# Performance work log

Hardware: AMD Instinct MI355X
Metric: run time of the kernel (lower is better)

Reference implementation:

```python
import jax, jax.numpy as jnp
import numpy as np
from jax import lax

DN = ('NCHW', 'OIHW', 'NCHW')

def _conv(x, w, b, stride, pad):
    o = lax.conv_general_dilated(x, w, (stride, stride), [(pad, pad), (pad, pad)], dimension_numbers=DN)
    return o + b[None, :, None, None]

def _conv_transpose(x, w, b, stride, pad):
    # w in torch ConvTranspose2d layout [Cin, Cout, kh, kw]
    k = w.shape[2]
    wf = jnp.flip(w, (2, 3)).transpose(1, 0, 2, 3)  # -> [Cout, Cin, kh, kw]
    p = k - 1 - pad
    o = lax.conv_general_dilated(x, wf, (1, 1), [(p, p), (p, p)], lhs_dilation=(stride, stride), dimension_numbers=DN)
    return o + b[None, :, None, None]

def setup_inputs() -> dict:
    key = jax.random.key(0)
    ks = jax.random.split(key, 16)
    s = 0.05
    NUM_EMB, EMB_DIM = 512, 128
    inp = {
        'x': jax.random.normal(ks[0], (32, 1, 224, 224), jnp.float32),
        # encoder
        'w_e1': jax.random.normal(ks[1], (64, 1, 4, 4), jnp.float32) * s,
        'b_e1': jnp.zeros((64,), jnp.float32),
        'w_e2': jax.random.normal(ks[2], (128, 64, 4, 4), jnp.float32) * s,
        'b_e2': jnp.zeros((128,), jnp.float32),
        'w_e3': jax.random.normal(ks[3], (128, 128, 3, 3), jnp.float32) * s,
        'b_e3': jnp.zeros((128,), jnp.float32),
        # codebook (torch init: uniform(-1/K, 1/K))
        'emb': jax.random.uniform(ks[4], (NUM_EMB, EMB_DIM), jnp.float32, -1.0 / NUM_EMB, 1.0 / NUM_EMB),
        # decoder
        'w_d1': jax.random.normal(ks[5], (128, 128, 3, 3), jnp.float32) * s,
        'b_d1': jnp.zeros((128,), jnp.float32),
        'w_dt1': jax.random.normal(ks[6], (128, 64, 4, 4), jnp.float32) * s,  # ConvTranspose [Cin,Cout,k,k]
        'b_dt1': jnp.zeros((64,), jnp.float32),
        'w_dt2': jax.random.normal(ks[7], (64, 1, 4, 4), jnp.float32) * s,
        'b_dt2': jnp.zeros((1,), jnp.float32),
    }
    return inp

def reference(x, w_e1, b_e1, w_e2, b_e2, w_e3, b_e3, emb, w_d1, b_d1, w_dt1, b_dt1, w_dt2, b_dt2):
    sg = lax.stop_gradient
    # --- encoder ---
    h = jax.nn.relu(_conv(x, w_e1, b_e1, 2, 1))
    h = jax.nn.relu(_conv(h, w_e2, b_e2, 2, 1))
    z_e = _conv(h, w_e3, b_e3, 1, 1)  # [B,128,H/4,W/4]
    B, C, H, W = z_e.shape
    # --- vector quantizer (faithful to source, incl. missing -2*z@e.T cross term) ---
    z_flat = z_e.transpose(0, 2, 3, 1).reshape(-1, C)  # [BHW, C]
    distances = (z_flat ** 2).sum(1, keepdims=True) + (emb ** 2).sum(1)  # [BHW, K]
    indices = jnp.argmin(distances, axis=1)
    z_q = emb[indices].reshape(B, H, W, C).transpose(0, 3, 1, 2)
    codebook_loss = jnp.mean((z_q - sg(z_e)) ** 2)
    commitment_loss = jnp.mean((sg(z_q) - z_e) ** 2)
    vq_loss = codebook_loss + commitment_loss
    # --- decoder ---
    d = _conv(z_q, w_d1, b_d1, 1, 1)
    d = jax.nn.relu(_conv_transpose(d, w_dt1, b_dt1, 2, 1))
    reconstructed_x = _conv_transpose(d, w_dt2, b_dt2, 2, 1)
    reconstruction_loss = jnp.mean((reconstructed_x - x) ** 2)
    total_loss = reconstruction_loss + vq_loss
    return (reconstructed_x, total_loss, reconstruction_loss, vq_loss)
```

## Files before the change

kernel.cpp:

```cpp
#include <hip/hip_runtime.h>
#include <hip/hip_bf16.h>

using bf16 = __hip_bfloat16;
using short8 = __attribute__((ext_vector_type(8))) short;
using f32x16 = __attribute__((ext_vector_type(16))) float;

__device__ __forceinline__ ushort f2us(float v) {
    bf16 h = __float2bfloat16(v);
    return *reinterpret_cast<ushort*>(&h);
}

#define MFMA32(a, b, c) __builtin_amdgcn_mfma_f32_32x32x16_bf16((a), (b), (c), 0, 0, 0)

__device__ __forceinline__ void gload16(const void* g, void* l) {
    __builtin_amdgcn_global_load_lds(
        (const __attribute__((address_space(1))) unsigned int*)g,
        (__attribute__((address_space(3))) unsigned int*)l, 16, 0, 0);
}

__device__ __forceinline__ int cls8(int i) {
    if (i == 0) return 0;
    if (i == 1) return 1;
    if (i == 2) return 2;
    if (i == 109) return 5;
    if (i == 110) return 6;
    if (i == 111) return 7;
    return (i & 1) ? 4 : 3;
}

__global__ void k_codebook(const float* __restrict__ emb, float* __restrict__ c) {
    __shared__ float sval[512];
    __shared__ int   sidx[512];
    int k = threadIdx.x;
    float s = 0.f;
    const float4* e4 = (const float4*)(emb + k * 128);
    #pragma unroll
    for (int d = 0; d < 32; ++d) {
        float4 v = e4[d];
        s += v.x * v.x + v.y * v.y + v.z * v.z + v.w * v.w;
    }
    sval[k] = s; sidx[k] = k;
    __syncthreads();
    for (int off = 256; off > 0; off >>= 1) {
        if (k < off) {
            float v2 = sval[k + off]; int i2 = sidx[k + off];
            if (v2 < sval[k] || (v2 == sval[k] && i2 < sidx[k])) { sval[k] = v2; sidx[k] = i2; }
        }
        __syncthreads();
    }
    int kmin = sidx[0];
    if (k < 128) c[k] = emb[kmin * 128 + k];
}

__global__ __launch_bounds__(256) void k_prepack(const float* __restrict__ w_e2,
                                                 const float* __restrict__ w_e3,
                                                 ushort* __restrict__ Wb2f,
                                                 ushort* __restrict__ Wb3f) {
    int i = blockIdx.x * 256 + threadIdx.x;
    const int n2 = 131072;
    const int n3 = 147456;
    if (i < n2) {
        int j = i & 7, l = (i >> 3) & 63, ks = (i >> 9) & 3, mf = (i >> 11) & 1,
            mh = (i >> 12) & 1, tap = i >> 13;
        int co = mh * 64 + mf * 32 + (l & 31);
        int ci = ks * 16 + (l >> 5) * 8 + j;
        int kh = tap >> 2, kw = tap & 3;
        Wb2f[i] = f2us(w_e2[((co * 64 + ci) * 4 + kh) * 4 + kw]);
    } else if (i < n2 + n3) {
        int t = i - n2;
        int j = t & 7, l = (t >> 3) & 63, ks = (t >> 9) & 7, mf = (t >> 12) & 1,
            mh = (t >> 13) & 1, tap = t >> 14;
        int co = mh * 64 + mf * 32 + (l & 31);
        int ci = ks * 16 + (l >> 5) * 8 + j;
        int kh = tap / 3, kw = tap % 3;
        Wb3f[t] = f2us(w_e3[((co * 128 + ci) * 3 + kh) * 3 + kw]);
    }
}

__global__ __launch_bounds__(256) void k_conv1(const float* __restrict__ x,
                                               const float* __restrict__ w,
                                               const float* __restrict__ bias,
                                               ushort* __restrict__ h1s) {
    __shared__ float wl[1024];
    __shared__ float bl[64];
    __shared__ __align__(16) char obuf[28672];
    int tid = threadIdx.x;
    for (int i = tid; i < 1024; i += 256) wl[i] = w[i];
    if (tid < 64) bl[tid] = bias[tid];
    __syncthreads();
    int r = blockIdx.x, b = blockIdx.y;
    int g = tid >> 6;
    int q = tid & 63;
    bool act = q < 56;
    int oh = 2 * r + (q >= 28);
    int ow0 = (q % 28) * 4;

    float xv[4][10];
    const float* xb = x + (size_t)b * 50176;
    #pragma unroll
    for (int kh = 0; kh < 4; ++kh) {
        int ih = 2 * oh - 1 + kh;
        bool rok = act && (unsigned)ih < 224u;
        #pragma unroll
        for (int j = 0; j < 10; ++j) {
            int iw = 2 * ow0 - 1 + j;
            xv[kh][j] = (rok && (unsigned)iw < 224u) ? xb[ih * 224 + iw] : 0.f;
        }
    }
    float a[4][16];
    #pragma unroll
    for (int i = 0; i < 4; ++i)
        #pragma unroll
        for (int j = 0; j < 16; ++j) a[i][j] = 0.f;

    const float4* wl4 = (const float4*)wl;
    #pragma unroll
    for (int j = 0; j < 16; ++j) {
        int co = g * 16 + j;
        #pragma unroll
        for (int kh = 0; kh < 4; ++kh) {
            float4 wr = wl4[co * 4 + kh];
            #pragma unroll
            for (int i = 0; i < 4; ++i) {
                a[i][j] += xv[kh][2*i+0]*wr.x + xv[kh][2*i+1]*wr.y
                         + xv[kh][2*i+2]*wr.z + xv[kh][2*i+3]*wr.w;
            }
        }
    }
    if (act) {
        #pragma unroll
        for (int i = 0; i < 4; ++i) {
            int ow = ow0 + i, wq = ow >> 1, pw = ow & 1;
            char* rowb = obuf + (oh & 1) * 14336 + wq * 256;
            int key = (wq & 15) << 4;
            #pragma unroll
            for (int j = 0; j < 16; ++j) {
                int co = g * 16 + j;
                *(ushort*)(rowb + ((pw * 128 + co * 2) ^ key)) =
                    f2us(fmaxf(a[i][j] + bl[co], 0.f));
            }
        }
    }
    __syncthreads();
    const float4* sb = (const float4*)obuf;
    for (int i = tid; i < 1792; i += 256) {
        int ph = (i >= 896) ? 1 : 0;
        float4* dst = (float4*)((char*)h1s + (((size_t)(b * 2 + ph)) * 56 + r) * 14336);
        dst[i - ph * 896] = sb[i];
    }
}

__global__ __launch_bounds__(256) void k_conv2_mfma(const ushort* __restrict__ h1s,
                                                    const ushort* __restrict__ Wb2f,
                                                    const float* __restrict__ bias,
                                                    ushort* __restrict__ h2s) {
    __shared__ __align__(16) char ldsc[6 * 14848 + 2 * 16384];
    int lin = blockIdx.x;
    int v = (lin & 7) * 112 + (lin >> 3);
    int b = v / 28, oh0 = (v % 28) * 2;
    int tid = threadIdx.x, lane = tid & 63, wv = tid >> 6;
    int mh = wv & 1, r = wv >> 1;
    int lrow = lane & 31, khalf = lane >> 5;
    const float4 z4 = {0.f, 0.f, 0.f, 0.f};

    if (tid < 192) {
        int s = tid >> 5, rr = (tid >> 4) & 1, col = tid & 15;
        ((float4*)(ldsc + s * 14848 + rr * 57 * 256))[col] = z4;
    }
    #pragma unroll
    for (int s = 0; s < 6; ++s) {
        int ph = (s < 3) ? 0 : 1;
        int rr = (s < 3) ? (oh0 + s) : (oh0 - 4 + s);
        char* ldst = ldsc + s * 14848 + 256;
        if ((unsigned)rr < 56u) {
            const char* src = (const char*)h1s + (((size_t)(b * 2 + ph)) * 56 + rr) * 14336;
            for (int c2 = wv; c2 < 14; c2 += 4)
                gload16(src + c2 * 1024 + lane * 16, ldst + c2 * 1024);
        } else {
            for (int i = tid; i < 896; i += 256) ((float4*)ldst)[i] = z4;
        }
    }
    {
        const char* asrc = (const char*)Wb2f;
        #pragma unroll
        for (int t = 0; t < 4; ++t)
            gload16(asrc + (wv * 4 + t) * 1024 + lane * 16,
                    ldsc + 89088 + (wv * 4 + t) * 1024);
    }
    __syncthreads();

    const f32x16 vz = {0,0,0,0,0,0,0,0,0,0,0,0,0,0,0,0};
    f32x16 acc[2][2];
    #pragma unroll
    for (int cf = 0; cf < 2; ++cf)
        #pragma unroll
        for (int mf = 0; mf < 2; ++mf) acc[cf][mf] = vz;

    #pragma unroll
    for (int tap = 0; tap < 16; ++tap) {
        const char* Acur = ldsc + 89088 + (tap & 1) * 16384;
        if (tap < 15) {
            char* Anxt = ldsc + 89088 + ((tap + 1) & 1) * 16384;
            const char* asrc = (const char*)Wb2f + (size_t)(tap + 1) * 16384;
            #pragma unroll
            for (int t = 0; t < 4; ++t)
                gload16(asrc + (wv * 4 + t) * 1024 + lane * 16,
                        Anxt + (wv * 4 + t) * 1024);
        }
        short8 af[2][4];
        #pragma unroll
        for (int mf = 0; mf < 2; ++mf)
            #pragma unroll
            for (int ks = 0; ks < 4; ++ks)
                af[mf][ks] = *(const short8*)(Acur + ((mh * 2 + mf) * 4 + ks) * 1024 + lane * 16);
        const int kh = tap >> 2, kw = tap & 3;
        const int pw = (kw & 1) ? 0 : 1;
        const int wofs = (kw == 0) ? 0 : (kw == 3) ? 2 : 1;
        const int sbase = (kh == 0) ? 3 : (kh == 1) ? 0 : (kh == 2) ? 4 : 1;
        const char* slab = ldsc + (sbase + r) * 14848;
        const int colb = pw * 128 + khalf * 16;
        #pragma unroll
        for (int cf = 0; cf < 2; ++cf) {
            int wp = cf * 24 + lrow + wofs;
            int key = ((wp - 1) & 15) << 4;
            const char* rowb = slab + wp * 256;
            #pragma unroll
            for (int ks = 0; ks < 4; ++ks) {
                short8 bv = *(const short8*)(rowb + ((colb + ks * 32) ^ key));
                acc[cf][0] = MFMA32(af[0][ks], bv, acc[cf][0]);
                acc[cf][1] = MFMA32(af[1][ks], bv, acc[cf][1]);
            }
        }
        __syncthreads();
    }
    {
        char* obuf = ldsc + r * 14336;
        #pragma unroll
        for (int cf = 0; cf < 2; ++cf) {
            int ow = cf * 24 + lrow;
            if (cf == 0 || lrow >= 8) {
                char* rowb = obuf + ow * 256;
                int key = (ow & 15) << 4;
                #pragma unroll
                for (int mf = 0; mf < 2; ++mf)
                    #pragma unroll
                    for (int reg = 0; reg < 16; ++reg) {
                        int co = mh * 64 + mf * 32 + (reg & 3) + 8 * (reg >> 2) + 4 * khalf;
                        float vv = fmaxf(acc[cf][mf][reg] + bias[co], 0.f);
                        *(ushort*)(rowb + ((co * 2) ^ key)) = f2us(vv);
                    }
            }
        }
    }
    __syncthreads();
    const float4* sb = (const float4*)ldsc;
    for (int i = tid; i < 1792; i += 256) {
        int rr = (i >= 896) ? 1 : 0;
        float4* dst = (float4*)((char*)h2s + ((size_t)(b * 56) + oh0 + rr) * 14336);
        dst[i - rr * 896] = sb[i];
    }
}

__global__ __launch_bounds__(512, 2) void k_conv3_mfma(const ushort* __restrict__ h2s,
                                                       const ushort* __restrict__ Wb3f,
                                                       const float* __restrict__ bias,
                                                       const float* __restrict__ c,
                                                       float* __restrict__ vq_part) {
    __shared__ __align__(16) char ldsc[6 * 14848 + 2 * 32768];
    __shared__ float red[8];
    int lin = blockIdx.x;
    int v = (lin & 7) * 56 + (lin >> 3);
    int b = v / 14, oh0 = (v % 14) * 4;
    int tid = threadIdx.x, lane = tid & 63, wv = tid >> 6;
    int mh = wv & 1, r = wv >> 1;
    int lrow = lane & 31, khalf = lane >> 5;
    const float4 z4 = {0.f, 0.f, 0.f, 0.f};

    if (tid < 192) {
        int s = tid >> 5, rr = (tid >> 4) & 1, col = tid & 15;
        ((float4*)(ldsc + s * 14848 + rr * 57 * 256))[col] = z4;
    }
    #pragma unroll
    for (int s = 0; s < 6; ++s) {
        int rr = oh0 - 1 + s;
        char* ldst = ldsc + s * 14848 + 256;
        if ((unsigned)rr < 56u) {
            const char* src = (const char*)h2s + ((size_t)b * 56 + rr) * 14336;
            for (int c2 = wv; c2 < 14; c2 += 8)
                gload16(src + c2 * 1024 + lane * 16, ldst + c2 * 1024);
        } else {
            for (int i = tid; i < 896; i += 512) ((float4*)ldst)[i] = z4;
        }
    }
    {
        const char* asrc = (const char*)Wb3f;
        #pragma unroll
        for (int t = 0; t < 4; ++t)
            gload16(asrc + (wv * 4 + t) * 1024 + lane * 16,
                    ldsc + 89088 + (wv * 4 + t) * 1024);
    }
    __syncthreads();

    const f32x16 vz = {0,0,0,0,0,0,0,0,0,0,0,0,0,0,0,0};
    f32x16 acc[2][2];
    #pragma unroll
    for (int cf = 0; cf < 2; ++cf)
        #pragma unroll
        for (int mf = 0; mf < 2; ++mf) acc[cf][mf] = vz;

    #pragma unroll
    for (int tap = 0; tap < 9; ++tap) {
        const char* Acur = ldsc + 89088 + (tap & 1) * 32768;
        if (tap < 8) {
            char* Anxt = ldsc + 89088 + ((tap + 1) & 1) * 32768;
            const char* asrc = (const char*)Wb3f + (size_t)(tap + 1) * 32768;
            #pragma unroll
            for (int t = 0; t < 4; ++t)
                gload16(asrc + (wv * 4 + t) * 1024 + lane * 16,
                        Anxt + (wv * 4 + t) * 1024);
        }
        short8 af[2][8];
        #pragma unroll
        for (int mf = 0; mf < 2; ++mf)
            #pragma unroll
            for (int ks = 0; ks < 8; ++ks)
                af[mf][ks] = *(const short8*)(Acur + ((mh * 2 + mf) * 8 + ks) * 1024 + lane * 16);
        const int kh = tap / 3, kw = tap % 3;
        const char* slab = ldsc + (r + kh) * 14848;
        #pragma unroll
        for (int cf = 0; cf < 2; ++cf) {
            int wp = cf * 24 + lrow + kw;
            int key = ((wp - 1) & 15) << 4;
            const char* rowb = slab + wp * 256;
            #pragma unroll
            for (int ks = 0; ks < 8; ++ks) {
                short8 bv = *(const short8*)(rowb + ((khalf * 16 + ks * 32) ^ key));
                acc[cf][0] = MFMA32(af[0][ks], bv, acc[cf][0]);
                acc[cf][1] = MFMA32(af[1][ks], bv, acc[cf][1]);
            }
        }
        __syncthreads();
    }
    float ls = 0.f;
    #pragma unroll
    for (int cf = 0; cf < 2; ++cf) {
        if (cf == 0 || lrow >= 8) {
            #pragma unroll
            for (int mf = 0; mf < 2; ++mf)
                #pragma unroll
                for (int reg = 0; reg < 16; ++reg) {
                    int co = mh * 64 + mf * 32 + (reg & 3) + 8 * (reg >> 2) + 4 * khalf;
                    float z = acc[cf][mf][reg] + bias[co];
                    float d = c[co] - z;
                    ls += d * d;
                }
        }
    }
    #pragma unroll
    for (int off = 32; off > 0; off >>= 1) ls += __shfl_down(ls, off);
    if (lane == 0) red[wv] = ls;
    __syncthreads();
    if (tid == 0) {
        float t = 0.f;
        #pragma unroll
        for (int i = 0; i < 8; ++i) t += red[i];
        vq_part[v] = t;
    }
}

__global__ __launch_bounds__(128) void k_SD3(const float* __restrict__ w_d1,
                                             const float* __restrict__ c,
                                             const float* __restrict__ b_d1,
                                             float* __restrict__ D3) {
    int co = blockIdx.x, ci = threadIdx.x;
    __shared__ float cl[128];
    __shared__ float part[9][128];
    cl[ci] = c[ci];
    __syncthreads();
    const float* wp = w_d1 + (co * 128 + ci) * 9;
    float cv = cl[ci];
    #pragma unroll
    for (int t = 0; t < 9; ++t) part[t][ci] = wp[t] * cv;
    __syncthreads();
    for (int off = 64; off > 0; off >>= 1) {
        if (ci < off) {
            #pragma unroll
            for (int t = 0; t < 9; ++t) part[t][ci] += part[t][ci + off];
        }
        __syncthreads();
    }
    if (ci < 9) {
        int rh = ci / 3, rw = ci % 3;
        int kh0 = (rh == 0) ? 1 : 0, kh1 = (rh == 2) ? 1 : 2;
        int kw0 = (rw == 0) ? 1 : 0, kw1 = (rw == 2) ? 1 : 2;
        float a = b_d1[co];
        for (int kh = kh0; kh <= kh1; ++kh)
            for (int kw = kw0; kw <= kw1; ++kw)
                a += part[kh * 3 + kw][0];
        D3[co * 9 + ci] = a;
    }
}

__global__ __launch_bounds__(64) void k_d2c(const float* __restrict__ D3,
                                            const float* __restrict__ w_dt1,
                                            const float* __restrict__ b_dt1,
                                            float* __restrict__ d2c) {
    __shared__ float dl[1152];
    int gh = blockIdx.x, gw = blockIdx.y, co2 = threadIdx.x;
    for (int i = co2; i < 1152; i += 64) dl[i] = D3[i];
    __syncthreads();
    const int rep[8] = {0, 1, 2, 4, 3, 109, 110, 111};
    int oh = rep[gh], ow = rep[gw];
    float a = b_dt1[co2];
    #pragma unroll
    for (int th = 0; th < 2; ++th) {
        int kh = ((oh + 1) & 1) + 2 * th;
        int ih = (oh + 1 - kh) >> 1;
        if ((unsigned)ih >= 56u) continue;
        int rh = (ih == 0) ? 0 : (ih == 55) ? 2 : 1;
        #pragma unroll
        for (int tw = 0; tw < 2; ++tw) {
            int kw = ((ow + 1) & 1) + 2 * tw;
            int iw = (ow + 1 - kw) >> 1;
            if ((unsigned)iw >= 56u) continue;
            int rw = (iw == 0) ? 0 : (iw == 55) ? 2 : 1;
            float t = 0.f;
            for (int ci = 0; ci < 128; ++ci)
                t += dl[ci * 9 + rh * 3 + rw] * w_dt1[(ci * 64 + co2) * 16 + kh * 4 + kw];
            a += t;
        }
    }
    d2c[(gh * 8 + gw) * 64 + co2] = fmaxf(a, 0.f);
}

__global__ __launch_bounds__(256) void k_Rbuild(const float* __restrict__ d2c,
                                                const float* __restrict__ w_dt2,
                                                const float* __restrict__ b_dt2,
                                                float* __restrict__ R) {
    __shared__ float el[1024];
    int tid = threadIdx.x;
    #pragma unroll
    for (int q = 0; q < 4; ++q) {
        int id = tid * 4 + q;
        int kh = id >> 8, kw = (id >> 6) & 3, gh = (id >> 3) & 7, gw = id & 7;
        float t = 0.f;
        const float* dp = d2c + (gh * 8 + gw) * 64;
        const float* wp = w_dt2 + kh * 4 + kw;
        for (int ci = 0; ci < 64; ++ci) t += dp[ci] * wp[ci * 16];
        el[((kh * 4 + kw) * 8 + gh) * 8 + gw] = t;
    }
    __syncthreads();
    int s = blockIdx.x * 256 + tid;
    int oh = s / 224, ow = s % 224;
    float a = b_dt2[0];
    #pragma unroll
    for (int th = 0; th < 2; ++th) {
        int kh = ((oh + 1) & 1) + 2 * th;
        int ih = (oh + 1 - kh) >> 1;
        if ((unsigned)ih >= 112u) continue;
        int ch = cls8(ih);
        #pragma unroll
        for (int tw = 0; tw < 2; ++tw) {
            int kw = ((ow + 1) & 1) + 2 * tw;
            int iw = (ow + 1 - kw) >> 1;
            if ((unsigned)iw >= 112u) continue;
            int cw = cls8(iw);
            a += el[((kh * 4 + kw) * 8 + ch) * 8 + cw];
        }
    }
    R[s] = a;
}

__global__ __launch_bounds__(256) void k_out(const float* __restrict__ R,
                                             const float* __restrict__ x,
                                             float* __restrict__ out,
                                             float* __restrict__ rec_part) {
    int base = blockIdx.x * 512 + threadIdx.x;
    float v = 0.f;
    #pragma unroll
    for (int t = 0; t < 2; ++t) {
        int i4 = base + t * 256;
        int s4 = i4 % 12544;
        float4 r = ((const float4*)R)[s4];
        float4 xv = ((const float4*)x)[i4];
        ((float4*)out)[i4] = r;
        float dx = r.x - xv.x, dy = r.y - xv.y, dz = r.z - xv.z, dw = r.w - xv.w;
        v += dx * dx + dy * dy + dz * dz + dw * dw;
    }
    __shared__ float red[4];
    #pragma unroll
    for (int off = 32; off > 0; off >>= 1) v += __shfl_down(v, off);
    int wid = threadIdx.x >> 6, lane = threadIdx.x & 63;
    if (lane == 0) red[wid] = v;
    __syncthreads();
    if (threadIdx.x == 0) rec_part[blockIdx.x] = red[0] + red[1] + red[2] + red[3];
}

__global__ __launch_bounds__(256) void k_fin(const float* __restrict__ vq_part,
                                             const float* __restrict__ rec_part,
                                             float* __restrict__ out, int loss_base) {
    __shared__ float sv[256], sr[256];
    float a = 0.f, b2 = 0.f;
    for (int i = threadIdx.x; i < 448; i += 256) a  += vq_part[i];
    for (int i = threadIdx.x; i < 784; i += 256) b2 += rec_part[i];
    sv[threadIdx.x] = a; sr[threadIdx.x] = b2;
    __syncthreads();
    for (int off = 128; off > 0; off >>= 1) {
        if (threadIdx.x < off) { sv[threadIdx.x] += sv[threadIdx.x + off]; sr[threadIdx.x] += sr[threadIdx.x + off]; }
        __syncthreads();
    }
    if (threadIdx.x == 0) {
        float vq  = 2.f * sv[0] / 12845056.f;
        float rec = sr[0] / 1605632.f;
        out[loss_base + 0] = rec + vq;
        out[loss_base + 1] = rec;
        out[loss_base + 2] = vq;
    }
}

extern "C" void kernel_launch(void* const* d_in, const int* in_sizes, int n_in,
                              void* d_out, int out_size, void* d_ws, size_t ws_size,
                              hipStream_t stream) {
    const float* x     = (const float*)d_in[0];
    const float* w_e1  = (const float*)d_in[1];
    const float* b_e1  = (const float*)d_in[2];
    const float* w_e2  = (const float*)d_in[3];
    const float* b_e2  = (const float*)d_in[4];
    const float* w_e3  = (const float*)d_in[5];
    const float* b_e3  = (const float*)d_in[6];
    const float* emb   = (const float*)d_in[7];
    const float* w_d1  = (const float*)d_in[8];
    const float* b_d1  = (const float*)d_in[9];
    const float* w_dt1 = (const float*)d_in[10];
    const float* b_dt1 = (const float*)d_in[11];
    const float* w_dt2 = (const float*)d_in[12];
    const float* b_dt2 = (const float*)d_in[13];
    float* out = (float*)d_out;
    float* ws  = (float*)d_ws;

    float* c        = ws + 16;
    float* D3       = ws + 256;
    float* d2c      = ws + 2048;
    float* R        = ws + 8192;
    float* vq_part  = ws + 65536;
    float* rec_part = ws + 67584;
    ushort* Wb2f    = (ushort*)(ws + 131072);
    ushort* Wb3f    = (ushort*)(ws + 196608);
    ushort* h1s     = (ushort*)(ws + 1310720);
    ushort* h2s     = (ushort*)(ws + 14155776);

    k_codebook<<<1, 512, 0, stream>>>(emb, c);
    k_prepack<<<1088, 256, 0, stream>>>(w_e2, w_e3, Wb2f, Wb3f);
    k_conv1<<<dim3(56, 32), 256, 0, stream>>>(x, w_e1, b_e1, h1s);
    k_conv2_mfma<<<896, 256, 0, stream>>>(h1s, Wb2f, b_e2, h2s);
    k_conv3_mfma<<<448, 512, 0, stream>>>(h2s, Wb3f, b_e3, c, vq_part);
    k_SD3<<<128, 128, 0, stream>>>(w_d1, c, b_d1, D3);
    k_d2c<<<dim3(8, 8), 64, 0, stream>>>(D3, w_dt1, b_dt1, d2c);
    k_Rbuild<<<196, 256, 0, stream>>>(d2c, w_dt2, b_dt2, R);
    k_out<<<784, 256, 0, stream>>>(R, x, out, rec_part);
    k_fin<<<1, 256, 0, stream>>>(vq_part, rec_part, out, out_size - 3);
}
```

Measured before the change: 185.7 us.

## Shrink conv2/conv3 blocks to one output row and single-buffer weights

```diff
diff --git a/kernel.cpp b/kernel.cpp
--- a/kernel.cpp
+++ b/kernel.cpp
@@ -154,23 +154,24 @@
                                                     const ushort* __restrict__ Wb2f,
                                                     const float* __restrict__ bias,
                                                     ushort* __restrict__ h2s) {
-    __shared__ __align__(16) char ldsc[6 * 14848 + 2 * 16384];
+    __shared__ __align__(16) char ldsc[4 * 14848 + 16384];
+    char* Ab = ldsc + 4 * 14848;
     int lin = blockIdx.x;
-    int v = (lin & 7) * 112 + (lin >> 3);
-    int b = v / 28, oh0 = (v % 28) * 2;
+    int v = (lin & 7) * 224 + (lin >> 3);
+    int b = v / 56, oh = v % 56;
     int tid = threadIdx.x, lane = tid & 63, wv = tid >> 6;
-    int mh = wv & 1, r = wv >> 1;
+    int mh = wv & 1, cf = wv >> 1;
     int lrow = lane & 31, khalf = lane >> 5;
     const float4 z4 = {0.f, 0.f, 0.f, 0.f};
 
-    if (tid < 192) {
+    if (tid < 128) {
         int s = tid >> 5, rr = (tid >> 4) & 1, col = tid & 15;
         ((float4*)(ldsc + s * 14848 + rr * 57 * 256))[col] = z4;
     }
     #pragma unroll
-    for (int s = 0; s < 6; ++s) {
-        int ph = (s < 3) ? 0 : 1;
-        int rr = (s < 3) ? (oh0 + s) : (oh0 - 4 + s);
+    for (int s = 0; s < 4; ++s) {
+        int ph = s >> 1;
+        int rr = (s == 0) ? oh : (s == 1) ? oh + 1 : (s == 2) ? oh - 1 : oh;
         char* ldst = ldsc + s * 14848 + 256;
         if ((unsigned)rr < 56u) {
             const char* src = (const char*)h1s + (((size_t)(b * 2 + ph)) * 56 + rr) * 14336;
@@ -181,191 +182,159 @@
         }
     }
     {
-        const char* asrc = (const char*)Wb2f;
         #pragma unroll
         for (int t = 0; t < 4; ++t)
-            gload16(asrc + (wv * 4 + t) * 1024 + lane * 16,
-                    ldsc + 89088 + (wv * 4 + t) * 1024);
+            gload16((const char*)Wb2f + (wv * 4 + t) * 1024 + lane * 16,
+                    Ab + (wv * 4 + t) * 1024);
     }
     __syncthreads();
 
     const f32x16 vz = {0,0,0,0,0,0,0,0,0,0,0,0,0,0,0,0};
-    f32x16 acc[2][2];
-    #pragma unroll
-    for (int cf = 0; cf < 2; ++cf)
-        #pragma unroll
-        for (int mf = 0; mf < 2; ++mf) acc[cf][mf] = vz;
+    f32x16 acc0 = vz, acc1 = vz;
 
     #pragma unroll
     for (int tap = 0; tap < 16; ++tap) {
-        const char* Acur = ldsc + 89088 + (tap & 1) * 16384;
+        short8 af[2][4];
+        #pragma unroll
+        for (int mf = 0; mf < 2; ++mf)
+            #pragma unroll
+            for (int ks = 0; ks < 4; ++ks)
+                af[mf][ks] = *(const short8*)(Ab + ((mh * 2 + mf) * 4 + ks) * 1024 + lane * 16);
+        __syncthreads();
         if (tap < 15) {
-            char* Anxt = ldsc + 89088 + ((tap + 1) & 1) * 16384;
             const char* asrc = (const char*)Wb2f + (size_t)(tap + 1) * 16384;
             #pragma unroll
             for (int t = 0; t < 4; ++t)
                 gload16(asrc + (wv * 4 + t) * 1024 + lane * 16,
-                        Anxt + (wv * 4 + t) * 1024);
-        }
-        short8 af[2][4];
-        #pragma unroll
-        for (int mf = 0; mf < 2; ++mf)
-            #pragma unroll
-            for (int ks = 0; ks < 4; ++ks)
-                af[mf][ks] = *(const short8*)(Acur + ((mh * 2 + mf) * 4 + ks) * 1024 + lane * 16);
+                        Ab + (wv * 4 + t) * 1024);
+        }
         const int kh = tap >> 2, kw = tap & 3;
         const int pw = (kw & 1) ? 0 : 1;
         const int wofs = (kw == 0) ? 0 : (kw == 3) ? 2 : 1;
-        const int sbase = (kh == 0) ? 3 : (kh == 1) ? 0 : (kh == 2) ? 4 : 1;
-        const char* slab = ldsc + (sbase + r) * 14848;
+        const int sidx = (kh == 0) ? 2 : (kh == 1) ? 0 : (kh == 2) ? 3 : 1;
+        const char* slab = ldsc + sidx * 14848;
         const int colb = pw * 128 + khalf * 16;
-        #pragma unroll
-        for (int cf = 0; cf < 2; ++cf) {
-            int wp = cf * 24 + lrow + wofs;
-            int key = ((wp - 1) & 15) << 4;
-            const char* rowb = slab + wp * 256;
-            #pragma unroll
-            for (int ks = 0; ks < 4; ++ks) {
-                short8 bv = *(const short8*)(rowb + ((colb + ks * 32) ^ key));
-                acc[cf][0] = MFMA32(af[0][ks], bv, acc[cf][0]);
-                acc[cf][1] = MFMA32(af[1][ks], bv, acc[cf][1]);
-            }
+        int wp = cf * 24 + lrow + wofs;
+        int key = ((wp - 1) & 15) << 4;
+        const char* rowb = slab + wp * 256;
+        #pragma unroll
+        for (int ks = 0; ks < 4; ++ks) {
+            short8 bv = *(const short8*)(rowb + ((colb + ks * 32) ^ key));
+            acc0 = MFMA32(af[0][ks], bv, acc0);
+            acc1 = MFMA32(af[1][ks], bv, acc1);
         }
         __syncthreads();
     }
     {
-        char* obuf = ldsc + r * 14336;
-        #pragma unroll
-        for (int cf = 0; cf < 2; ++cf) {
-            int ow = cf * 24 + lrow;
-            if (cf == 0 || lrow >= 8) {
-                char* rowb = obuf + ow * 256;
-                int key = (ow & 15) << 4;
-                #pragma unroll
-                for (int mf = 0; mf < 2; ++mf)
-                    #pragma unroll
-                    for (int reg = 0; reg < 16; ++reg) {
-                        int co = mh * 64 + mf * 32 + (reg & 3) + 8 * (reg >> 2) + 4 * khalf;
-                        float vv = fmaxf(acc[cf][mf][reg] + bias[co], 0.f);
-                        *(ushort*)(rowb + ((co * 2) ^ key)) = f2us(vv);
-                    }
-            }
-        }
-    }
-    __syncthreads();
-    const float4* sb = (const float4*)ldsc;
-    for (int i = tid; i < 1792; i += 256) {
-        int rr = (i >= 896) ? 1 : 0;
-        float4* dst = (float4*)((char*)h2s + ((size_t)(b * 56) + oh0 + rr) * 14336);
-        dst[i - rr * 896] = sb[i];
-    }
-}
-
-__global__ __launch_bounds__(512, 2) void k_conv3_mfma(const ushort* __restrict__ h2s,
-                                                       const ushort* __restrict__ Wb3f,
-                                                       const float* __restrict__ bias,
-                                                       const float* __restrict__ c,
-                                                       float* __restrict__ vq_part) {
-    __shared__ __align__(16) char ldsc[6 * 14848 + 2 * 32768];
-    __shared__ float red[8];
-    int lin = blockIdx.x;
-    int v = (lin & 7) * 56 + (lin >> 3);
-    int b = v / 14, oh0 = (v % 14) * 4;
-    int tid = threadIdx.x, lane = tid & 63, wv = tid >> 6;
-    int mh = wv & 1, r = wv >> 1;
-    int lrow = lane & 31, khalf = lane >> 5;
-    const float4 z4 = {0.f, 0.f, 0.f, 0.f};
-
-    if (tid < 192) {
-        int s = tid >> 5, rr = (tid >> 4) & 1, col = tid & 15;
-        ((float4*)(ldsc + s * 14848 + rr * 57 * 256))[col] = z4;
-    }
-    #pragma unroll
-    for (int s = 0; s < 6; ++s) {
-        int rr = oh0 - 1 + s;
-        char* ldst = ldsc + s * 14848 + 256;
-        if ((unsigned)rr < 56u) {
-            const char* src = (const char*)h2s + ((size_t)b * 56 + rr) * 14336;
-            for (int c2 = wv; c2 < 14; c2 += 8)
-                gload16(src + c2 * 1024 + lane * 16, ldst + c2 * 1024);
-        } else {
-            for (int i = tid; i < 896; i += 512) ((float4*)ldst)[i] = z4;
-        }
-    }
-    {
-        const char* asrc = (const char*)Wb3f;
-        #pragma unroll
-        for (int t = 0; t < 4; ++t)
-            gload16(asrc + (wv * 4 + t) * 1024 + lane * 16,
-                    ldsc + 89088 + (wv * 4 + t) * 1024);
-    }
-    __syncthreads();
-
-    const f32x16 vz = {0,0,0,0,0,0,0,0,0,0,0,0,0,0,0,0};
-    f32x16 acc[2][2];
-    #pragma unroll
-    for (int cf = 0; cf < 2; ++cf)
-        #pragma unroll
-        for (int mf = 0; mf < 2; ++mf) acc[cf][mf] = vz;
-
-    #pragma unroll
-    for (int tap = 0; tap < 9; ++tap) {
-        const char* Acur = ldsc + 89088 + (tap & 1) * 32768;
-        if (tap < 8) {
-            char* Anxt = ldsc + 89088 + ((tap + 1) & 1) * 32768;
-            const char* asrc = (const char*)Wb3f + (size_t)(tap + 1) * 32768;
-            #pragma unroll
-            for (int t = 0; t < 4; ++t)
-                gload16(asrc + (wv * 4 + t) * 1024 + lane * 16,
-                        Anxt + (wv * 4 + t) * 1024);
-        }
-        short8 af[2][8];
-        #pragma unroll
-        for (int mf = 0; mf < 2; ++mf)
-            #pragma unroll
-            for (int ks = 0; ks < 8; ++ks)
-                af[mf][ks] = *(const short8*)(Acur + ((mh * 2 + mf) * 8 + ks) * 1024 + lane * 16);
-        const int kh = tap / 3, kw = tap % 3;
-        const char* slab = ldsc + (r + kh) * 14848;
-        #pragma unroll
-        for (int cf = 0; cf < 2; ++cf) {
-            int wp = cf * 24 + lrow + kw;
-            int key = ((wp - 1) & 15) << 4;
-            const char* rowb = slab + wp * 256;
-            #pragma unroll
-            for (int ks = 0; ks < 8; ++ks) {
-                short8 bv = *(const short8*)(rowb + ((khalf * 16 + ks * 32) ^ key));
-                acc[cf][0] = MFMA32(af[0][ks], bv, acc[cf][0]);
-                acc[cf][1] = MFMA32(af[1][ks], bv, acc[cf][1]);
-            }
-        }
-        __syncthreads();
-    }
-    float ls = 0.f;
-    #pragma unroll
-    for (int cf = 0; cf < 2; ++cf) {
+        int ow = cf * 24 + lrow;
         if (cf == 0 || lrow >= 8) {
+            char* rowb = ldsc + ow * 256;
+            int key = (ow & 15) << 4;
             #pragma unroll
             for (int mf = 0; mf < 2; ++mf)
                 #pragma unroll
                 for (int reg = 0; reg < 16; ++reg) {
                     int co = mh * 64 + mf * 32 + (reg & 3) + 8 * (reg >> 2) + 4 * khalf;
-                    float z = acc[cf][mf][reg] + bias[co];
-                    float d = c[co] - z;
-                    ls += d * d;
+                    float vv = fmaxf((mf ? acc1[reg] : acc0[reg]) + bias[co], 0.f);
+                    *(ushort*)(rowb + ((co * 2) ^ key)) = f2us(vv);
                 }
         }
+    }
+    __syncthreads();
+    const float4* sb = (const float4*)ldsc;
+    float4* dst = (float4*)((char*)h2s + ((size_t)b * 56 + oh) * 14336);
+    for (int i = tid; i < 896; i += 256) dst[i] = sb[i];
+}
+
+__global__ __launch_bounds__(256) void k_conv3_mfma(const ushort* __restrict__ h2s,
+                                                    const ushort* __restrict__ Wb3f,
+                                                    const float* __restrict__ bias,
+                                                    const float* __restrict__ c,
+                                                    float* __restrict__ vq_part) {
+    __shared__ __align__(16) char ldsc[3 * 14848 + 32768];
+    char* Ab = ldsc + 3 * 14848;
+    __shared__ float red[4];
+    int lin = blockIdx.x;
+    int v = (lin & 7) * 224 + (lin >> 3);
+    int b = v / 56, oh = v % 56;
+    int tid = threadIdx.x, lane = tid & 63, wv = tid >> 6;
+    int mh = wv & 1, cf = wv >> 1;
+    int lrow = lane & 31, khalf = lane >> 5;
+    const float4 z4 = {0.f, 0.f, 0.f, 0.f};
+
+    if (tid < 96) {
+        int s = tid >> 5, rr = (tid >> 4) & 1, col = tid & 15;
+        ((float4*)(ldsc + s * 14848 + rr * 57 * 256))[col] = z4;
+    }
+    #pragma unroll
+    for (int s = 0; s < 3; ++s) {
+        int rr = oh - 1 + s;
+        char* ldst = ldsc + s * 14848 + 256;
+        if ((unsigned)rr < 56u) {
+            const char* src = (const char*)h2s + ((size_t)b * 56 + rr) * 14336;
+            for (int c2 = wv; c2 < 14; c2 += 4)
+                gload16(src + c2 * 1024 + lane * 16, ldst + c2 * 1024);
+        } else {
+            for (int i = tid; i < 896; i += 256) ((float4*)ldst)[i] = z4;
+        }
+    }
+    {
+        #pragma unroll
+        for (int t = 0; t < 8; ++t)
+            gload16((const char*)Wb3f + (wv * 8 + t) * 1024 + lane * 16,
+                    Ab + (wv * 8 + t) * 1024);
+    }
+    __syncthreads();
+
+    const f32x16 vz = {0,0,0,0,0,0,0,0,0,0,0,0,0,0,0,0};
+    f32x16 acc0 = vz, acc1 = vz;
+
+    #pragma unroll
+    for (int tap = 0; tap < 9; ++tap) {
+        short8 af[2][8];
+        #pragma unroll
+        for (int mf = 0; mf < 2; ++mf)
+            #pragma unroll
+            for (int ks = 0; ks < 8; ++ks)
+                af[mf][ks] = *(const short8*)(Ab + ((mh * 2 + mf) * 8 + ks) * 1024 + lane * 16);
+        __syncthreads();
+        if (tap < 8) {
+            const char* asrc = (const char*)Wb3f + (size_t)(tap + 1) * 32768;
+            #pragma unroll
+            for (int t = 0; t < 8; ++t)
+                gload16(asrc + (wv * 8 + t) * 1024 + lane * 16,
+                        Ab + (wv * 8 + t) * 1024);
+        }
+        const int kh = tap / 3, kw = tap % 3;
+        const char* slab = ldsc + kh * 14848;
+        int wp = cf * 24 + lrow + kw;
+        int key = ((wp - 1) & 15) << 4;
+        const char* rowb = slab + wp * 256;
+        #pragma unroll
+        for (int ks = 0; ks < 8; ++ks) {
+            short8 bv = *(const short8*)(rowb + ((khalf * 16 + ks * 32) ^ key));
+            acc0 = MFMA32(af[0][ks], bv, acc0);
+            acc1 = MFMA32(af[1][ks], bv, acc1);
+        }
+        __syncthreads();
+    }
+    float ls = 0.f;
+    if (cf == 0 || lrow >= 8) {
+        #pragma unroll
+        for (int mf = 0; mf < 2; ++mf)
+            #pragma unroll
+            for (int reg = 0; reg < 16; ++reg) {
+                int co = mh * 64 + mf * 32 + (reg & 3) + 8 * (reg >> 2) + 4 * khalf;
+                float z = (mf ? acc1[reg] : acc0[reg]) + bias[co];
+                float d = c[co] - z;
+                ls += d * d;
+            }
     }
     #pragma unroll
     for (int off = 32; off > 0; off >>= 1) ls += __shfl_down(ls, off);
     if (lane == 0) red[wv] = ls;
     __syncthreads();
-    if (tid == 0) {
-        float t = 0.f;
-        #pragma unroll
-        for (int i = 0; i < 8; ++i) t += red[i];
-        vq_part[v] = t;
-    }
+    if (tid == 0) vq_part[v] = red[0] + red[1] + red[2] + red[3];
 }
 
 __global__ __launch_bounds__(128) void k_SD3(const float* __restrict__ w_d1,
@@ -501,8 +470,8 @@
                                              float* __restrict__ out, int loss_base) {
     __shared__ float sv[256], sr[256];
     float a = 0.f, b2 = 0.f;
-    for (int i = threadIdx.x; i < 448; i += 256) a  += vq_part[i];
-    for (int i = threadIdx.x; i < 784; i += 256) b2 += rec_part[i];
+    for (int i = threadIdx.x; i < 1792; i += 256) a  += vq_part[i];
+    for (int i = threadIdx.x; i < 784;  i += 256) b2 += rec_part[i];
     sv[threadIdx.x] = a; sr[threadIdx.x] = b2;
     __syncthreads();
     for (int off = 128; off > 0; off >>= 1) {
@@ -543,7 +512,7 @@
     float* d2c      = ws + 2048;
     float* R        = ws + 8192;
     float* vq_part  = ws + 65536;
-    float* rec_part = ws + 67584;
+    float* rec_part = ws + 69632;
     ushort* Wb2f    = (ushort*)(ws + 131072);
     ushort* Wb3f    = (ushort*)(ws + 196608);
     ushort* h1s     = (ushort*)(ws + 1310720);
@@ -552,8 +521,8 @@
     k_codebook<<<1, 512, 0, stream>>>(emb, c);
     k_prepack<<<1088, 256, 0, stream>>>(w_e2, w_e3, Wb2f, Wb3f);
     k_conv1<<<dim3(56, 32), 256, 0, stream>>>(x, w_e1, b_e1, h1s);
-    k_conv2_mfma<<<896, 256, 0, stream>>>(h1s, Wb2f, b_e2, h2s);
-    k_conv3_mfma<<<448, 512, 0, stream>>>(h2s, Wb3f, b_e3, c, vq_part);
+    k_conv2_mfma<<<1792, 256, 0, stream>>>(h1s, Wb2f, b_e2, h2s);
+    k_conv3_mfma<<<1792, 256, 0, stream>>>(h2s, Wb3f, b_e3, c, vq_part);
     k_SD3<<<128, 128, 0, stream>>>(w_d1, c, b_d1, D3);
     k_d2c<<<dim3(8, 8), 64, 0, stream>>>(D3, w_dt1, b_dt1, d2c);
     k_Rbuild<<<196, 256, 0, stream>>>(d2c, w_dt2, b_dt2, R);
```

Measured after the change: 196.1 us. 1.06x slower.

## Drop per-tap block barriers in conv2, retile conv3 with triple buffering, fuse Rbuild

Applied to the files above, without the earlier changes.

```diff
diff --git a/kernel.cpp b/kernel.cpp
--- a/kernel.cpp
+++ b/kernel.cpp
@@ -154,7 +154,8 @@
                                                     const ushort* __restrict__ Wb2f,
                                                     const float* __restrict__ bias,
                                                     ushort* __restrict__ h2s) {
-    __shared__ __align__(16) char ldsc[6 * 14848 + 2 * 16384];
+    __shared__ __align__(16) char ldsc[6 * 14848 + 4 * 16384];
+    char* ldsA = ldsc + 89088;
     int lin = blockIdx.x;
     int v = (lin & 7) * 112 + (lin >> 3);
     int b = v / 28, oh0 = (v % 28) * 2;
@@ -180,12 +181,12 @@
             for (int i = tid; i < 896; i += 256) ((float4*)ldst)[i] = z4;
         }
     }
+    char* Aown = ldsA + wv * 16384;
+    const char* Wbase = (const char*)Wb2f;
     {
-        const char* asrc = (const char*)Wb2f;
-        #pragma unroll
-        for (int t = 0; t < 4; ++t)
-            gload16(asrc + (wv * 4 + t) * 1024 + lane * 16,
-                    ldsc + 89088 + (wv * 4 + t) * 1024);
+        #pragma unroll
+        for (int p = 0; p < 8; ++p)
+            gload16(Wbase + mh * 8192 + p * 1024 + lane * 16, Aown + p * 1024);
     }
     __syncthreads();
 
@@ -198,21 +199,24 @@
 
     #pragma unroll
     for (int tap = 0; tap < 16; ++tap) {
-        const char* Acur = ldsc + 89088 + (tap & 1) * 16384;
         if (tap < 15) {
-            char* Anxt = ldsc + 89088 + ((tap + 1) & 1) * 16384;
-            const char* asrc = (const char*)Wb2f + (size_t)(tap + 1) * 16384;
-            #pragma unroll
-            for (int t = 0; t < 4; ++t)
-                gload16(asrc + (wv * 4 + t) * 1024 + lane * 16,
-                        Anxt + (wv * 4 + t) * 1024);
-        }
+            const char* asrc = Wbase + (size_t)(tap + 1) * 16384 + mh * 8192;
+            char* dst = Aown + ((tap + 1) & 1) * 8192;
+            #pragma unroll
+            for (int p = 0; p < 8; ++p)
+                gload16(asrc + p * 1024 + lane * 16, dst + p * 1024);
+            asm volatile("s_waitcnt vmcnt(8)" ::: "memory");
+        } else {
+            asm volatile("s_waitcnt vmcnt(0)" ::: "memory");
+        }
+        __builtin_amdgcn_sched_barrier(0);
+        const char* Acur = Aown + (tap & 1) * 8192;
         short8 af[2][4];
         #pragma unroll
         for (int mf = 0; mf < 2; ++mf)
             #pragma unroll
             for (int ks = 0; ks < 4; ++ks)
-                af[mf][ks] = *(const short8*)(Acur + ((mh * 2 + mf) * 4 + ks) * 1024 + lane * 16);
+                af[mf][ks] = *(const short8*)(Acur + (mf * 4 + ks) * 1024 + lane * 16);
         const int kh = tap >> 2, kw = tap & 3;
         const int pw = (kw & 1) ? 0 : 1;
         const int wofs = (kw == 0) ? 0 : (kw == 3) ? 2 : 1;
@@ -231,8 +235,8 @@
                 acc[cf][1] = MFMA32(af[1][ks], bv, acc[cf][1]);
             }
         }
-        __syncthreads();
-    }
+    }
+    __syncthreads();
     {
         char* obuf = ldsc + r * 14336;
         #pragma unroll
@@ -261,43 +265,46 @@
     }
 }
 
-__global__ __launch_bounds__(512, 2) void k_conv3_mfma(const ushort* __restrict__ h2s,
-                                                       const ushort* __restrict__ Wb3f,
-                                                       const float* __restrict__ bias,
-                                                       const float* __restrict__ c,
-                                                       float* __restrict__ vq_part) {
-    __shared__ __align__(16) char ldsc[6 * 14848 + 2 * 32768];
-    __shared__ float red[8];
+__global__ __launch_bounds__(256) void k_conv3_mfma(const ushort* __restrict__ h2s,
+                                                    const ushort* __restrict__ Wb3f,
+                                                    const float* __restrict__ bias,
+                                                    const float* __restrict__ c,
+                                                    float* __restrict__ vq_part) {
+    __shared__ __align__(16) char ldsc[4 * 14848 + 3 * 32768];
+    __shared__ float red[4];
+    char* ldsA = ldsc + 59392;
     int lin = blockIdx.x;
-    int v = (lin & 7) * 56 + (lin >> 3);
-    int b = v / 14, oh0 = (v % 14) * 4;
+    int v = (lin & 7) * 112 + (lin >> 3);
+    int b = v / 28, oh0 = (v % 28) * 2;
     int tid = threadIdx.x, lane = tid & 63, wv = tid >> 6;
     int mh = wv & 1, r = wv >> 1;
     int lrow = lane & 31, khalf = lane >> 5;
     const float4 z4 = {0.f, 0.f, 0.f, 0.f};
 
-    if (tid < 192) {
+    if (tid < 128) {
         int s = tid >> 5, rr = (tid >> 4) & 1, col = tid & 15;
         ((float4*)(ldsc + s * 14848 + rr * 57 * 256))[col] = z4;
     }
     #pragma unroll
-    for (int s = 0; s < 6; ++s) {
+    for (int s = 0; s < 4; ++s) {
         int rr = oh0 - 1 + s;
         char* ldst = ldsc + s * 14848 + 256;
         if ((unsigned)rr < 56u) {
             const char* src = (const char*)h2s + ((size_t)b * 56 + rr) * 14336;
-            for (int c2 = wv; c2 < 14; c2 += 8)
+            for (int c2 = wv; c2 < 14; c2 += 4)
                 gload16(src + c2 * 1024 + lane * 16, ldst + c2 * 1024);
         } else {
-            for (int i = tid; i < 896; i += 512) ((float4*)ldst)[i] = z4;
-        }
-    }
+            for (int i = tid; i < 896; i += 256) ((float4*)ldst)[i] = z4;
+        }
+    }
+    const char* Wbase = (const char*)Wb3f;
     {
-        const char* asrc = (const char*)Wb3f;
-        #pragma unroll
-        for (int t = 0; t < 4; ++t)
-            gload16(asrc + (wv * 4 + t) * 1024 + lane * 16,
-                    ldsc + 89088 + (wv * 4 + t) * 1024);
+        #pragma unroll
+        for (int t0 = 0; t0 < 2; ++t0)
+            #pragma unroll
+            for (int p = 0; p < 8; ++p)
+                gload16(Wbase + (size_t)t0 * 32768 + (wv * 8 + p) * 1024 + lane * 16,
+                        ldsA + t0 * 32768 + (wv * 8 + p) * 1024);
     }
     __syncthreads();
 
@@ -310,15 +317,14 @@
 
     #pragma unroll
     for (int tap = 0; tap < 9; ++tap) {
-        const char* Acur = ldsc + 89088 + (tap & 1) * 32768;
-        if (tap < 8) {
-            char* Anxt = ldsc + 89088 + ((tap + 1) & 1) * 32768;
-            const char* asrc = (const char*)Wb3f + (size_t)(tap + 1) * 32768;
-            #pragma unroll
-            for (int t = 0; t < 4; ++t)
-                gload16(asrc + (wv * 4 + t) * 1024 + lane * 16,
-                        Anxt + (wv * 4 + t) * 1024);
-        }
+        if (tap < 7) {
+            const char* asrc = Wbase + (size_t)(tap + 2) * 32768;
+            char* dst = ldsA + ((tap + 2) % 3) * 32768;
+            #pragma unroll
+            for (int p = 0; p < 8; ++p)
+                gload16(asrc + (wv * 8 + p) * 1024 + lane * 16, dst + (wv * 8 + p) * 1024);
+        }
+        const char* Acur = ldsA + (tap % 3) * 32768;
         short8 af[2][8];
         #pragma unroll
         for (int mf = 0; mf < 2; ++mf)
@@ -339,7 +345,15 @@
                 acc[cf][1] = MFMA32(af[1][ks], bv, acc[cf][1]);
             }
         }
-        __syncthreads();
+        if (tap < 7) {
+            asm volatile("s_waitcnt vmcnt(8)" ::: "memory");
+            __builtin_amdgcn_s_barrier();
+            __builtin_amdgcn_sched_barrier(0);
+        } else if (tap == 7) {
+            asm volatile("s_waitcnt vmcnt(0)" ::: "memory");
+            __builtin_amdgcn_s_barrier();
+            __builtin_amdgcn_sched_barrier(0);
+        }
     }
     float ls = 0.f;
     #pragma unroll
@@ -360,12 +374,7 @@
     for (int off = 32; off > 0; off >>= 1) ls += __shfl_down(ls, off);
     if (lane == 0) red[wv] = ls;
     __syncthreads();
-    if (tid == 0) {
-        float t = 0.f;
-        #pragma unroll
-        for (int i = 0; i < 8; ++i) t += red[i];
-        vq_part[v] = t;
-    }
+    if (tid == 0) vq_part[v] = red[0] + red[1] + red[2] + red[3];
 }
 
 __global__ __launch_bounds__(128) void k_SD3(const float* __restrict__ w_d1,
@@ -433,10 +442,12 @@
     d2c[(gh * 8 + gw) * 64 + co2] = fmaxf(a, 0.f);
 }
 
-__global__ __launch_bounds__(256) void k_Rbuild(const float* __restrict__ d2c,
-                                                const float* __restrict__ w_dt2,
-                                                const float* __restrict__ b_dt2,
-                                                float* __restrict__ R) {
+__global__ __launch_bounds__(256) void k_out(const float* __restrict__ d2c,
+                                             const float* __restrict__ w_dt2,
+                                             const float* __restrict__ b_dt2,
+                                             const float* __restrict__ x,
+                                             float* __restrict__ out,
+                                             float* __restrict__ rec_part) {
     __shared__ float el[1024];
     int tid = threadIdx.x;
     #pragma unroll
@@ -450,38 +461,38 @@
         el[((kh * 4 + kw) * 8 + gh) * 8 + gw] = t;
     }
     __syncthreads();
-    int s = blockIdx.x * 256 + tid;
-    int oh = s / 224, ow = s % 224;
-    float a = b_dt2[0];
-    #pragma unroll
-    for (int th = 0; th < 2; ++th) {
-        int kh = ((oh + 1) & 1) + 2 * th;
-        int ih = (oh + 1 - kh) >> 1;
-        if ((unsigned)ih >= 112u) continue;
-        int ch = cls8(ih);
-        #pragma unroll
-        for (int tw = 0; tw < 2; ++tw) {
-            int kw = ((ow + 1) & 1) + 2 * tw;
-            int iw = (ow + 1 - kw) >> 1;
-            if ((unsigned)iw >= 112u) continue;
-            int cw = cls8(iw);
-            a += el[((kh * 4 + kw) * 8 + ch) * 8 + cw];
-        }
-    }
-    R[s] = a;
-}
-
-__global__ __launch_bounds__(256) void k_out(const float* __restrict__ R,
-                                             const float* __restrict__ x,
-                                             float* __restrict__ out,
-                                             float* __restrict__ rec_part) {
-    int base = blockIdx.x * 512 + threadIdx.x;
+    float bb = b_dt2[0];
+    int base = blockIdx.x * 512 + tid;
     float v = 0.f;
     #pragma unroll
-    for (int t = 0; t < 2; ++t) {
-        int i4 = base + t * 256;
+    for (int t2 = 0; t2 < 2; ++t2) {
+        int i4 = base + t2 * 256;
         int s4 = i4 % 12544;
-        float4 r = ((const float4*)R)[s4];
+        int p0 = s4 * 4;
+        int oh = p0 / 224, ow0 = p0 % 224;
+        float rv[4];
+        #pragma unroll
+        for (int j = 0; j < 4; ++j) {
+            int ow = ow0 + j;
+            float a = bb;
+            #pragma unroll
+            for (int th = 0; th < 2; ++th) {
+                int kh = ((oh + 1) & 1) + 2 * th;
+                int ih = (oh + 1 - kh) >> 1;
+                if ((unsigned)ih < 112u) {
+                    int ch = cls8(ih);
+                    #pragma unroll
+                    for (int tw = 0; tw < 2; ++tw) {
+                        int kw = ((ow + 1) & 1) + 2 * tw;
+                        int iw = (ow + 1 - kw) >> 1;
+                        if ((unsigned)iw < 112u)
+                            a += el[((kh * 4 + kw) * 8 + ch) * 8 + cls8(iw)];
+                    }
+                }
+            }
+            rv[j] = a;
+        }
+        float4 r; r.x = rv[0]; r.y = rv[1]; r.z = rv[2]; r.w = rv[3];
         float4 xv = ((const float4*)x)[i4];
         ((float4*)out)[i4] = r;
         float dx = r.x - xv.x, dy = r.y - xv.y, dz = r.z - xv.z, dw = r.w - xv.w;
@@ -490,10 +501,10 @@
     __shared__ float red[4];
     #pragma unroll
     for (int off = 32; off > 0; off >>= 1) v += __shfl_down(v, off);
-    int wid = threadIdx.x >> 6, lane = threadIdx.x & 63;
+    int wid = tid >> 6, lane = tid & 63;
     if (lane == 0) red[wid] = v;
     __syncthreads();
-    if (threadIdx.x == 0) rec_part[blockIdx.x] = red[0] + red[1] + red[2] + red[3];
+    if (tid == 0) rec_part[blockIdx.x] = red[0] + red[1] + red[2] + red[3];
 }
 
 __global__ __launch_bounds__(256) void k_fin(const float* __restrict__ vq_part,
@@ -501,7 +512,7 @@
                                              float* __restrict__ out, int loss_base) {
     __shared__ float sv[256], sr[256];
     float a = 0.f, b2 = 0.f;
-    for (int i = threadIdx.x; i < 448; i += 256) a  += vq_part[i];
+    for (int i = threadIdx.x; i < 896; i += 256) a  += vq_part[i];
     for (int i = threadIdx.x; i < 784; i += 256) b2 += rec_part[i];
     sv[threadIdx.x] = a; sr[threadIdx.x] = b2;
     __syncthreads();
@@ -541,9 +552,8 @@
     float* c        = ws + 16;
     float* D3       = ws + 256;
     float* d2c      = ws + 2048;
-    float* R        = ws + 8192;
     float* vq_part  = ws + 65536;
-    float* rec_part = ws + 67584;
+    float* rec_part = ws + 69632;
     ushort* Wb2f    = (ushort*)(ws + 131072);
     ushort* Wb3f    = (ushort*)(ws + 196608);
     ushort* h1s     = (ushort*)(ws + 1310720);
@@ -553,10 +563,9 @@
     k_prepack<<<1088, 256, 0, stream>>>(w_e2, w_e3, Wb2f, Wb3f);
     k_conv1<<<dim3(56, 32), 256, 0, stream>>>(x, w_e1, b_e1, h1s);
     k_conv2_mfma<<<896, 256, 0, stream>>>(h1s, Wb2f, b_e2, h2s);
-    k_conv3_mfma<<<448, 512, 0, stream>>>(h2s, Wb3f, b_e3, c, vq_part);
+    k_conv3_mfma<<<896, 256, 0, stream>>>(h2s, Wb3f, b_e3, c, vq_part);
     k_SD3<<<128, 128, 0, stream>>>(w_d1, c, b_d1, D3);
     k_d2c<<<dim3(8, 8), 64, 0, stream>>>(D3, w_dt1, b_dt1, d2c);
-    k_Rbuild<<<196, 256, 0, stream>>>(d2c, w_dt2, b_dt2, R);
-    k_out<<<784, 256, 0, stream>>>(R, x, out, rec_part);
+    k_out<<<784, 256, 0, stream>>>(d2c, w_dt2, b_dt2, x, out, rec_part);
     k_fin<<<1, 256, 0, stream>>>(vq_part, rec_part, out, out_size - 3);
 }
```

New measurement: 227.8 us. 1.23x slower.
